# Kernel tuning notes

Hardware: AMD Instinct MI355X
Metric: run time of the kernel (lower is better)

## Reference

```python
import jax, jax.numpy as jnp
import numpy as np

MIDC = 256
HEADS = 8
HEADC = MIDC // HEADS
EPS = 1e-5


def _ln(x, gamma, beta):
    # LayerNorm over last dim (headc)
    mu = jnp.mean(x, axis=-1, keepdims=True)
    var = jnp.var(x, axis=-1, keepdims=True)
    return (x - mu) * jax.lax.rsqrt(var + EPS) * gamma + beta


def setup_inputs() -> dict:
    key = jax.random.key(0)
    ks = jax.random.split(key, 8)
    B, HW, C = 8, 4096, MIDC
    s = 1.0 / np.sqrt(C)
    return {
        "x": jax.random.normal(ks[0], (B, HW, C), jnp.float32),
        "w_qkv": jax.random.normal(ks[1], (C, 3 * C), jnp.float32) * s,
        "b_qkv": jnp.zeros((3 * C,), jnp.float32),
        "kln_g": jnp.ones((HEADC,), jnp.float32),
        "kln_b": jnp.zeros((HEADC,), jnp.float32),
        "vln_g": jnp.ones((HEADC,), jnp.float32),
        "vln_b": jnp.zeros((HEADC,), jnp.float32),
        "w1": jax.random.normal(ks[2], (C, C), jnp.float32) * s,
        "b1": jnp.zeros((C,), jnp.float32),
        "w2": jax.random.normal(ks[3], (C, C), jnp.float32) * s,
        "b2": jnp.zeros((C,), jnp.float32),
    }


def reference(x, w_qkv, b_qkv, kln_g, kln_b, vln_g, vln_b, w1, b1, w2, b2):
    B, HW, C = x.shape
    bias = x
    qkv = (x @ w_qkv + b_qkv).reshape(B, HW, HEADS, 3 * HEADC)
    qkv = qkv.transpose(0, 2, 1, 3)  # [B, h, HW, 3*headc]
    q, k, v = jnp.split(qkv, 3, axis=-1)  # each [B, h, HW, headc]
    k = _ln(k, kln_g, kln_b)
    v = _ln(v, vln_g, vln_b)
    # linear attention: (k^T v)/HW then q @ (.)
    kv = jnp.einsum('bhnd,bhne->bhde', k, v) / HW  # [B, h, headc, headc]
    out = jnp.einsum('bhnd,bhde->bhne', q, kv)     # [B, h, HW, headc]
    out = out.transpose(0, 2, 1, 3).reshape(B, HW, C)
    ret = out + bias
    # GELU MLP (torch nn.GELU default = exact erf form)
    h = jax.nn.gelu(ret @ w1 + b1, approximate=False)
    return h @ w2 + b2 + bias
```

## Files before the change

### kernel.cpp

```cpp
#include <hip/hip_runtime.h>
#include <hip/hip_bf16.h>
#include <math.h>

typedef _Float16 f16;
typedef _Float16 f16x4 __attribute__((ext_vector_type(4)));
typedef _Float16 f16x8 __attribute__((ext_vector_type(8)));
typedef float f32x4 __attribute__((ext_vector_type(4)));

#define MIDC 256
#define NHEADS 8
#define HEADC 32
#define HW_ 4096
#define BATCH 8
#define NTOK (BATCH*HW_)

__device__ __forceinline__ void gload_lds16(const void* g, void* lds){
    __builtin_amdgcn_global_load_lds(
        (const __attribute__((address_space(1))) unsigned int*)g,
        (__attribute__((address_space(3))) unsigned int*)lds, 16, 0, 0);
}

__global__ void k_f32_to_f16(const float* __restrict__ in, f16* __restrict__ out, int n){
    int i = (blockIdx.x*blockDim.x + threadIdx.x)*4;
    if (i < n) {
        float4 v = *reinterpret_cast<const float4*>(in + i);
        f16x4 o = { (f16)v.x, (f16)v.y, (f16)v.z, (f16)v.w };
        *reinterpret_cast<f16x4*>(out + i) = o;
    }
}

__global__ void k_prep(const float* __restrict__ wqkv, const float* __restrict__ w1,
                       const float* __restrict__ w2, const float* __restrict__ bq,
                       f16* __restrict__ wqkvT, f16* __restrict__ w1T,
                       f16* __restrict__ w2T, float* __restrict__ pb){
    int idx = blockIdx.x*blockDim.x + threadIdx.x;
    if (idx < 196608){
        int r = idx / 768, o = idx % 768;
        int h = o / 96, rr = o % 96, p = rr >> 5, d = o & 31;
        int n = (p << 8) + (h << 5) + d;
        wqkvT[(size_t)n*256 + r] = (f16)wqkv[idx];
    } else if (idx < 262144){
        int i = idx - 196608; int r = i >> 8, c = i & 255;
        w1T[(size_t)c*256 + r] = (f16)w1[i];
    } else if (idx < 327680){
        int i = idx - 262144; int r = i >> 8, c = i & 255;
        w2T[(size_t)c*256 + r] = (f16)w2[i];
    } else if (idx < 328448){
        int n = idx - 327680;
        int p = n >> 8, h = (n & 255) >> 5, d = n & 31;
        pb[n] = bq[h*96 + p*32 + d];
    }
}

__global__ __launch_bounds__(256) void k_gemm0(
    const f16* __restrict__ A, const f16* __restrict__ Bt,
    const float* __restrict__ bias,
    const float* __restrict__ kg_, const float* __restrict__ kb_,
    const float* __restrict__ vg_, const float* __restrict__ vb_,
    f16* __restrict__ oq, f16* __restrict__ ok, f16* __restrict__ ov)
{
    constexpr int K = 256;
    __shared__ __attribute__((aligned(16))) char smem[50176];
    f16* const AsB[2] = { (f16*)(smem),        (f16*)(smem+16384) };
    f16* const BsB[2] = { (f16*)(smem+8192),   (f16*)(smem+24576) };

    const int tid  = threadIdx.x;
    const int lane = tid & 63, wid = tid >> 6;

    const int nwg  = 6 * 256;
    const int orig = blockIdx.x + 6*blockIdx.y;
    const int lin  = (orig & 7) * (nwg >> 3) + (orig >> 3);
    const int bx = lin % 6, by = lin / 6;
    const int m0 = by * 128, n0 = bx * 128;

    const int wm = (wid >> 1) * 64, wn = (wid & 1) * 64;
    const int lr = lane & 15, kg = lane >> 4;

    f32x4 acc[4][4];
    #pragma unroll
    for (int i=0;i<4;i++)
        #pragma unroll
        for (int j=0;j<4;j++) acc[i][j] = (f32x4){0.f,0.f,0.f,0.f};

    const int srow = tid >> 2, scol = (tid & 3) * 8;
    const f16* gA = A  + (size_t)(m0 + srow)*K + scol;
    const f16* gB = Bt + (size_t)(n0 + srow)*K + scol;
    const size_t rstep = (size_t)64*K;

    auto STAGE = [&](int b, int kt){
        f16* ab = AsB[b] + wid*512;
        f16* bb = BsB[b] + wid*512;
        gload_lds16(gA + kt,          ab);
        gload_lds16(gA + kt + rstep,  ab + 2048);
        gload_lds16(gB + kt,          bb);
        gload_lds16(gB + kt + rstep,  bb + 2048);
    };

    STAGE(0, 0);
    __syncthreads();
    #pragma unroll
    for (int t = 0; t < 8; ++t){
        const int cur = t & 1;
        if (t < 7) STAGE(cur ^ 1, (t+1)*32);
        const f16* Ac = AsB[cur];
        const f16* Bc = BsB[cur];
        f16x8 a[4], b[4];
        #pragma unroll
        for (int fr=0; fr<4; fr++) a[fr] = *reinterpret_cast<const f16x8*>(Ac + (wm + fr*16 + lr)*32 + kg*8);
        #pragma unroll
        for (int fc=0; fc<4; fc++) b[fc] = *reinterpret_cast<const f16x8*>(Bc + (wn + fc*16 + lr)*32 + kg*8);
        #pragma unroll
        for (int fr=0; fr<4; fr++)
            #pragma unroll
            for (int fc=0; fc<4; fc++)
                acc[fr][fc] = __builtin_amdgcn_mfma_f32_16x16x32_f16(a[fr], b[fc], acc[fr][fc], 0, 0, 0);
        __syncthreads();
    }

    f16* Cs = (f16*)(smem + 16384);
    float bv[4];
    #pragma unroll
    for (int fc=0; fc<4; fc++) bv[fc] = bias[n0 + wn + fc*16 + lr];
    #pragma unroll
    for (int fr=0; fr<4; fr++)
    #pragma unroll
    for (int fc=0; fc<4; fc++)
    #pragma unroll
    for (int r=0; r<4; r++){
        float v = acc[fr][fc][r] + bv[fc];
        Cs[(wm + fr*16 + kg*4 + r)*132 + (wn + fc*16 + lr)] = (f16)v;
    }
    __syncthreads();
    int part = n0 >> 8;
    #pragma unroll
    for (int i=0;i<2;i++){
        int c = tid + i*256;
        int row = c >> 2, hc = c & 3;
        const f16* src = Cs + row*132 + hc*32;
        f16x8 d0 = *reinterpret_cast<const f16x8*>(src);
        f16x8 d1 = *reinterpret_cast<const f16x8*>(src + 8);
        f16x8 d2 = *reinterpret_cast<const f16x8*>(src + 16);
        f16x8 d3 = *reinterpret_cast<const f16x8*>(src + 24);
        int col0 = n0 + hc*32;
        int h = (col0 & 255) >> 5;
        int gm = m0 + row, b = gm >> 12, n = gm & 4095;
        f16* dst = (part==0 ? oq : (part==1 ? ok : ov))
                 + ((size_t)(b*NHEADS + h)*HW_ + n)*HEADC;
        if (part == 0){
            *reinterpret_cast<f16x8*>(dst)      = d0;
            *reinterpret_cast<f16x8*>(dst + 8)  = d1;
            *reinterpret_cast<f16x8*>(dst + 16) = d2;
            *reinterpret_cast<f16x8*>(dst + 24) = d3;
        } else {
            float vals[32];
            #pragma unroll
            for (int j=0;j<8;j++){
                vals[j]    = (float)d0[j];
                vals[8+j]  = (float)d1[j];
                vals[16+j] = (float)d2[j];
                vals[24+j] = (float)d3[j];
            }
            float s = 0.f, s2 = 0.f;
            #pragma unroll
            for (int j=0;j<32;j++){ s += vals[j]; s2 = fmaf(vals[j], vals[j], s2); }
            float mu  = s * (1.0f/32.0f);
            float var = s2 * (1.0f/32.0f) - mu*mu;
            float rs  = rsqrtf(var + 1e-5f);
            const float* gp = (part==1) ? kg_ : vg_;
            const float* bp = (part==1) ? kb_ : vb_;
            f16x8 o0, o1, o2, o3;
            #pragma unroll
            for (int j=0;j<8;j++){
                o0[j] = (f16)((vals[j]    - mu)*rs*gp[j]    + bp[j]);
                o1[j] = (f16)((vals[8+j]  - mu)*rs*gp[8+j]  + bp[8+j]);
                o2[j] = (f16)((vals[16+j] - mu)*rs*gp[16+j] + bp[16+j]);
                o3[j] = (f16)((vals[24+j] - mu)*rs*gp[24+j] + bp[24+j]);
            }
            *reinterpret_cast<f16x8*>(dst)      = o0;
            *reinterpret_cast<f16x8*>(dst + 8)  = o1;
            *reinterpret_cast<f16x8*>(dst + 16) = o2;
            *reinterpret_cast<f16x8*>(dst + 24) = o3;
        }
    }
}

template<int MODE>
__global__ __launch_bounds__(256, 4) void k_mlp(
    const f16* __restrict__ A, const f16* __restrict__ Bt,
    const float* __restrict__ bias,
    f16* __restrict__ oh,
    const f16* __restrict__ residh, float* __restrict__ of)
{
    constexpr int K = 256;
    __shared__ __attribute__((aligned(16))) char smem[24576];

    const int tid  = threadIdx.x;
    const int lane = tid & 63, wid = tid >> 6;

    const int nwg  = 4 * 256;
    const int orig = blockIdx.x + 4*blockIdx.y;
    const int lin  = (orig & 7) * (nwg >> 3) + (orig >> 3);
    const int bx = lin & 3, by = lin >> 2;
    const int m0 = by * 128, n0 = bx * 64;

    const int wm = (wid >> 1) * 64;
    const int wn = (wid & 1) * 32;
    const int lr = lane & 15, kg = lane >> 4;

    f32x4 acc[4][2];
    #pragma unroll
    for (int i=0;i<4;i++)
        #pragma unroll
        for (int j=0;j<2;j++) acc[i][j] = (f32x4){0.f,0.f,0.f,0.f};

    const int srow = tid >> 2, scol = (tid & 3) * 8;
    const f16* gA = A  + (size_t)(m0 + srow)*K + scol;
    const f16* gB = Bt + (size_t)(n0 + srow)*K + scol;

    auto STAGE = [&](int b, int kt){
        f16* Ab = (f16*)(smem + b*12288);
        f16* Bb = Ab + 4096;
        gload_lds16(gA + kt,                 Ab + wid*512);
        gload_lds16(gA + kt + (size_t)64*K,  Ab + 2048 + wid*512);
        gload_lds16(gB + kt,                 Bb + wid*512);
    };

    STAGE(0, 0);
    __syncthreads();
    #pragma unroll
    for (int t = 0; t < 8; ++t){
        const int cur = t & 1;
        if (t < 7) STAGE(cur ^ 1, (t+1)*32);
        const f16* Ab = (const f16*)(smem + cur*12288);
        const f16* Bb = Ab + 4096;
        f16x8 a[4], bf[2];
        #pragma unroll
        for (int fr=0; fr<4; fr++) a[fr]  = *reinterpret_cast<const f16x8*>(Ab + (wm + fr*16 + lr)*32 + kg*8);
        #pragma unroll
        for (int fc=0; fc<2; fc++) bf[fc] = *reinterpret_cast<const f16x8*>(Bb + (wn + fc*16 + lr)*32 + kg*8);
        #pragma unroll
        for (int fr=0; fr<4; fr++)
            #pragma unroll
            for (int fc=0; fc<2; fc++)
                acc[fr][fc] = __builtin_amdgcn_mfma_f32_16x16x32_f16(a[fr], bf[fc], acc[fr][fc], 0, 0, 0);
        __syncthreads();
    }

    float bv[2];
    #pragma unroll
    for (int fc=0; fc<2; fc++) bv[fc] = bias[n0 + wn + fc*16 + lr];

    if constexpr (MODE == 1){
        f16* Cs = (f16*)smem;
        #pragma unroll
        for (int fr=0; fr<4; fr++)
        #pragma unroll
        for (int fc=0; fc<2; fc++)
        #pragma unroll
        for (int r=0; r<4; r++){
            float v = acc[fr][fc][r] + bv[fc];
            v = 0.5f * v * (1.0f + erff(v * 0.70710678f));
            Cs[(wm + fr*16 + kg*4 + r)*72 + (wn + fc*16 + lr)] = (f16)v;
        }
        __syncthreads();
        int row = tid >> 1, ch = tid & 1;
        const f16* src = Cs + row*72 + ch*32;
        f16x8 d0 = *reinterpret_cast<const f16x8*>(src);
        f16x8 d1 = *reinterpret_cast<const f16x8*>(src + 8);
        f16x8 d2 = *reinterpret_cast<const f16x8*>(src + 16);
        f16x8 d3 = *reinterpret_cast<const f16x8*>(src + 24);
        f16* dst = oh + (size_t)(m0 + row)*MIDC + n0 + ch*32;
        *reinterpret_cast<f16x8*>(dst)      = d0;
        *reinterpret_cast<f16x8*>(dst + 8)  = d1;
        *reinterpret_cast<f16x8*>(dst + 16) = d2;
        *reinterpret_cast<f16x8*>(dst + 24) = d3;
    } else {
        #pragma unroll
        for (int fr=0; fr<4; fr++)
        #pragma unroll
        for (int fc=0; fc<2; fc++)
        #pragma unroll
        for (int r=0; r<4; r++){
            int gm = m0 + wm + fr*16 + kg*4 + r;
            int gn = n0 + wn + fc*16 + lr;
            size_t xi = (size_t)gm*MIDC + gn;
            of[xi] = acc[fr][fc][r] + bv[fc] + (float)residh[xi];
        }
    }
}

__global__ __launch_bounds__(256) void k_kv(const f16* __restrict__ kb, const f16* __restrict__ vb,
                                            float* __restrict__ kvpart){
    __shared__ __attribute__((aligned(16))) f16 ks[4][64][32];
    __shared__ __attribute__((aligned(16))) f16 vs[4][64][32];
    __shared__ __attribute__((aligned(16))) float red[4][32][32];
    const int bh = blockIdx.x, chunk = blockIdx.y;
    const int tid = threadIdx.x, lane = tid & 63, wid = tid >> 6;
    const int d0 = (lane >> 3) * 4, e0 = (lane & 7) * 4;
    const int tok0 = chunk*256 + wid*64;

    const f16* kg = kb + ((size_t)bh*HW_ + tok0)*HEADC;
    const f16* vg = vb + ((size_t)bh*HW_ + tok0)*HEADC;
    f16* ksw = &ks[wid][0][0]; f16* vsw = &vs[wid][0][0];
    #pragma unroll
    for (int i=0;i<4;i++){
        gload_lds16(kg + (size_t)(i*16 + (lane>>2))*HEADC + (lane&3)*8, ksw + i*512);
        gload_lds16(vg + (size_t)(i*16 + (lane>>2))*HEADC + (lane&3)*8, vsw + i*512);
    }
    __syncthreads();

    f32x4 acc[4];
    #pragma unroll
    for (int i=0;i<4;i++) acc[i] = (f32x4){0.f,0.f,0.f,0.f};
    #pragma unroll 4
    for (int t=0; t<64; t++){
        f16x4 kk = *reinterpret_cast<const f16x4*>(&ks[wid][t][d0]);
        f16x4 vv = *reinterpret_cast<const f16x4*>(&vs[wid][t][e0]);
        f32x4 vf = { (float)vv[0], (float)vv[1], (float)vv[2], (float)vv[3] };
        #pragma unroll
        for (int i=0;i<4;i++) acc[i] += (float)kk[i] * vf;
    }
    __syncthreads();
    #pragma unroll
    for (int i=0;i<4;i++) *reinterpret_cast<f32x4*>(&red[wid][d0+i][e0]) = acc[i];
    __syncthreads();
    int de0 = tid * 4;
    const float* rf = &red[0][0][0];
    f32x4 s = *reinterpret_cast<const f32x4*>(rf + de0);
    #pragma unroll
    for (int w=1; w<4; w++) s += *reinterpret_cast<const f32x4*>(rf + w*1024 + de0);
    *reinterpret_cast<f32x4*>(kvpart + ((size_t)bh*16 + chunk)*1024 + de0) = s;
}

__global__ void k_kvred(const float* __restrict__ kvpart, f16* __restrict__ kvT){
    int gid = blockIdx.x*blockDim.x + threadIdx.x;
    int bh = gid >> 10, de = gid & 1023;
    int d = de >> 5, e = de & 31;
    float s = 0.f;
    #pragma unroll
    for (int p=0; p<16; p++) s += kvpart[((size_t)bh*16 + p)*1024 + de];
    kvT[((size_t)bh << 10) + (e << 5) + d] = (f16)(s * (1.0f/4096.0f));
}

__global__ __launch_bounds__(256) void k_attn(const f16* __restrict__ qb, const f16* __restrict__ kvT,
                                              const f16* __restrict__ xb, f16* __restrict__ ret){
    __shared__ __attribute__((aligned(16))) f16 Ls[128][40];
    const int bh = blockIdx.x, chunk = blockIdx.y;
    const int b = bh >> 3, h = bh & 7;
    const int tid = threadIdx.x, lane = tid & 63, wid = tid >> 6;
    const int lr = lane & 15, kg = lane >> 4;
    const int row0 = chunk*128 + wid*32;

    f32x4 acc[2][2];
    #pragma unroll
    for (int i=0;i<2;i++)
        #pragma unroll
        for (int j=0;j<2;j++) acc[i][j] = (f32x4){0.f,0.f,0.f,0.f};

    f16x8 a[2], bb[2];
    #pragma unroll
    for (int fr=0; fr<2; fr++)
        a[fr] = *reinterpret_cast<const f16x8*>(qb + ((size_t)bh*HW_ + row0 + fr*16 + lr)*HEADC + kg*8);
    #pragma unroll
    for (int fc=0; fc<2; fc++)
        bb[fc] = *reinterpret_cast<const f16x8*>(kvT + ((size_t)bh << 10) + (size_t)(fc*16 + lr)*32 + kg*8);
    #pragma unroll
    for (int fr=0; fr<2; fr++)
        #pragma unroll
        for (int fc=0; fc<2; fc++)
            acc[fr][fc] = __builtin_amdgcn_mfma_f32_16x16x32_f16(a[fr], bb[fc], acc[fr][fc], 0, 0, 0);

    #pragma unroll
    for (int fr=0; fr<2; fr++)
    #pragma unroll
    for (int fc=0; fc<2; fc++)
    #pragma unroll
    for (int r=0; r<4; r++)
        Ls[wid*32 + fr*16 + kg*4 + r][fc*16 + lr] = (f16)acc[fr][fc][r];
    __syncthreads();

    int row = tid >> 1, hf = tid & 1;
    size_t base = ((size_t)b*HW_ + chunk*128 + row)*MIDC + h*HEADC + hf*16;
    f16x8 x0 = *reinterpret_cast<const f16x8*>(xb + base);
    f16x8 x1 = *reinterpret_cast<const f16x8*>(xb + base + 8);
    f16x8 s0 = *reinterpret_cast<const f16x8*>(&Ls[row][hf*16]);
    f16x8 s1 = *reinterpret_cast<const f16x8*>(&Ls[row][hf*16 + 8]);
    f16x8 o0, o1;
    #pragma unroll
    for (int j=0;j<8;j++){
        o0[j] = (f16)((float)s0[j] + (float)x0[j]);
        o1[j] = (f16)((float)s1[j] + (float)x1[j]);
    }
    *reinterpret_cast<f16x8*>(ret + base)     = o0;
    *reinterpret_cast<f16x8*>(ret + base + 8) = o1;
}

extern "C" void kernel_launch(void* const* d_in, const int* in_sizes, int n_in,
                              void* d_out, int out_size, void* d_ws, size_t ws_size,
                              hipStream_t stream) {
    const float* x     = (const float*)d_in[0];
    const float* w_qkv = (const float*)d_in[1];
    const float* b_qkv = (const float*)d_in[2];
    const float* kln_g = (const float*)d_in[3];
    const float* kln_b = (const float*)d_in[4];
    const float* vln_g = (const float*)d_in[5];
    const float* vln_b = (const float*)d_in[6];
    const float* w1    = (const float*)d_in[7];
    const float* b1    = (const float*)d_in[8];
    const float* w2    = (const float*)d_in[9];
    const float* b2    = (const float*)d_in[10];
    float* out = (float*)d_out;

    char* ws = (char*)d_ws;
    size_t off = 0;
    auto alloc = [&](size_t bytes) -> void* {
        void* p = ws + off; off += (bytes + 255) & ~255ULL; return p;
    };
    const size_t TOKB = (size_t)NTOK*MIDC*sizeof(f16);
    f16* xb    = (f16*)alloc(TOKB);
    f16* wqkvT = (f16*)alloc(768*256*sizeof(f16));
    f16* w1T   = (f16*)alloc(256*256*sizeof(f16));
    f16* w2T   = (f16*)alloc(256*256*sizeof(f16));
    float* pb  = (float*)alloc(768*sizeof(float));
    f16* qb    = (f16*)alloc(TOKB);
    f16* kb    = (f16*)alloc(TOKB);
    f16* vb    = (f16*)alloc(TOKB);
    float* kvpart = (float*)alloc((size_t)64*16*1024*sizeof(float));
    f16* kvT   = (f16*)alloc((size_t)64*1024*sizeof(f16));
    f16* retb = vb;
    f16* hb   = kb;

    k_f32_to_f16<<<dim3((NTOK*MIDC)/4/256), 256, 0, stream>>>(x, xb, NTOK*MIDC);
    k_prep<<<dim3((328448+255)/256), 256, 0, stream>>>(w_qkv, w1, w2, b_qkv, wqkvT, w1T, w2T, pb);

    k_gemm0<<<dim3(6, NTOK/128), 256, 0, stream>>>(
        xb, wqkvT, pb, kln_g, kln_b, vln_g, vln_b, qb, kb, vb);

    k_kv<<<dim3(64, HW_/256), 256, 0, stream>>>(kb, vb, kvpart);
    k_kvred<<<dim3(65536/256), 256, 0, stream>>>(kvpart, kvT);

    k_attn<<<dim3(64, HW_/128), 256, 0, stream>>>(qb, kvT, xb, retb);

    k_mlp<1><<<dim3(4, NTOK/128), 256, 0, stream>>>(
        retb, w1T, b1, hb, nullptr, nullptr);

    k_mlp<2><<<dim3(4, NTOK/128), 256, 0, stream>>>(
        hb, w2T, b2, nullptr, xb, out);
}
```

Measured before the change: 200.0 us.

## Merge prep kernels, fold kv reduction into attention, shrink LDS footprint

Combines the x conversion and weight-prep kernels into one launch, and removes the separate kv reduction kernel by having each attention block sum the 16 partial kv tiles itself into LDS. It also shrinks LDS in the QKV GEMM (epilogue staged in two halves reusing the operand buffers) and in k_kv (reduction buffer aliased over operand storage) to allow more resident workgroups. The aim is fewer launches and higher occupancy. The cost is that each attention block redundantly re-reads and reduces 64KB of partials (32 blocks per head), and the GEMM epilogue gains an extra barrier.

Result: faster. 193.7 us (-3.2%).

```diff
diff --git a/kernel.cpp b/kernel.cpp
--- a/kernel.cpp
+++ b/kernel.cpp
@@ -20,35 +20,35 @@
         (__attribute__((address_space(3))) unsigned int*)lds, 16, 0, 0);
 }
 
-__global__ void k_f32_to_f16(const float* __restrict__ in, f16* __restrict__ out, int n){
-    int i = (blockIdx.x*blockDim.x + threadIdx.x)*4;
-    if (i < n) {
-        float4 v = *reinterpret_cast<const float4*>(in + i);
+__global__ void k_init(const float* __restrict__ x, const float* __restrict__ wqkv,
+                       const float* __restrict__ w1, const float* __restrict__ w2,
+                       const float* __restrict__ bq,
+                       f16* __restrict__ xb, f16* __restrict__ wqkvT,
+                       f16* __restrict__ w1T, f16* __restrict__ w2T, float* __restrict__ pb){
+    int t = blockIdx.x*blockDim.x + threadIdx.x;
+    if (t < 2097152){
+        int i = t*4;
+        float4 v = *reinterpret_cast<const float4*>(x + i);
         f16x4 o = { (f16)v.x, (f16)v.y, (f16)v.z, (f16)v.w };
-        *reinterpret_cast<f16x4*>(out + i) = o;
-    }
-}
-
-__global__ void k_prep(const float* __restrict__ wqkv, const float* __restrict__ w1,
-                       const float* __restrict__ w2, const float* __restrict__ bq,
-                       f16* __restrict__ wqkvT, f16* __restrict__ w1T,
-                       f16* __restrict__ w2T, float* __restrict__ pb){
-    int idx = blockIdx.x*blockDim.x + threadIdx.x;
-    if (idx < 196608){
-        int r = idx / 768, o = idx % 768;
-        int h = o / 96, rr = o % 96, p = rr >> 5, d = o & 31;
-        int n = (p << 8) + (h << 5) + d;
-        wqkvT[(size_t)n*256 + r] = (f16)wqkv[idx];
-    } else if (idx < 262144){
-        int i = idx - 196608; int r = i >> 8, c = i & 255;
-        w1T[(size_t)c*256 + r] = (f16)w1[i];
-    } else if (idx < 327680){
-        int i = idx - 262144; int r = i >> 8, c = i & 255;
-        w2T[(size_t)c*256 + r] = (f16)w2[i];
-    } else if (idx < 328448){
-        int n = idx - 327680;
-        int p = n >> 8, h = (n & 255) >> 5, d = n & 31;
-        pb[n] = bq[h*96 + p*32 + d];
+        *reinterpret_cast<f16x4*>(xb + i) = o;
+    } else {
+        int j = t - 2097152;
+        if (j < 196608){
+            int r = j / 768, o = j % 768;
+            int h = o / 96, rr = o % 96, p = rr >> 5, d = o & 31;
+            int n = (p << 8) + (h << 5) + d;
+            wqkvT[(size_t)n*256 + r] = (f16)wqkv[j];
+        } else if (j < 262144){
+            int i2 = j - 196608; int r = i2 >> 8, c = i2 & 255;
+            w1T[(size_t)c*256 + r] = (f16)w1[i2];
+        } else if (j < 327680){
+            int i2 = j - 262144; int r = i2 >> 8, c = i2 & 255;
+            w2T[(size_t)c*256 + r] = (f16)w2[i2];
+        } else if (j < 328448){
+            int n = j - 327680;
+            int p = n >> 8, h = (n & 255) >> 5, d = n & 31;
+            pb[n] = bq[h*96 + p*32 + d];
+        }
     }
 }
 
@@ -60,9 +60,7 @@
     f16* __restrict__ oq, f16* __restrict__ ok, f16* __restrict__ ov)
 {
     constexpr int K = 256;
-    __shared__ __attribute__((aligned(16))) char smem[50176];
-    f16* const AsB[2] = { (f16*)(smem),        (f16*)(smem+16384) };
-    f16* const BsB[2] = { (f16*)(smem+8192),   (f16*)(smem+24576) };
+    __shared__ __attribute__((aligned(16))) char smem[32768];
 
     const int tid  = threadIdx.x;
     const int lane = tid & 63, wid = tid >> 6;
@@ -88,8 +86,9 @@
     const size_t rstep = (size_t)64*K;
 
     auto STAGE = [&](int b, int kt){
-        f16* ab = AsB[b] + wid*512;
-        f16* bb = BsB[b] + wid*512;
+        f16* base = (f16*)smem + b*8192;
+        f16* ab = base + wid*512;
+        f16* bb = base + 4096 + wid*512;
         gload_lds16(gA + kt,          ab);
         gload_lds16(gA + kt + rstep,  ab + 2048);
         gload_lds16(gB + kt,          bb);
@@ -102,8 +101,8 @@
     for (int t = 0; t < 8; ++t){
         const int cur = t & 1;
         if (t < 7) STAGE(cur ^ 1, (t+1)*32);
-        const f16* Ac = AsB[cur];
-        const f16* Bc = BsB[cur];
+        const f16* Ac = (const f16*)smem + cur*8192;
+        const f16* Bc = Ac + 4096;
         f16x8 a[4], b[4];
         #pragma unroll
         for (int fr=0; fr<4; fr++) a[fr] = *reinterpret_cast<const f16x8*>(Ac + (wm + fr*16 + lr)*32 + kg*8);
@@ -117,33 +116,36 @@
         __syncthreads();
     }
 
-    f16* Cs = (f16*)(smem + 16384);
+    f16* Cs = (f16*)smem;
     float bv[4];
     #pragma unroll
     for (int fc=0; fc<4; fc++) bv[fc] = bias[n0 + wn + fc*16 + lr];
-    #pragma unroll
-    for (int fr=0; fr<4; fr++)
-    #pragma unroll
-    for (int fc=0; fc<4; fc++)
-    #pragma unroll
-    for (int r=0; r<4; r++){
-        float v = acc[fr][fc][r] + bv[fc];
-        Cs[(wm + fr*16 + kg*4 + r)*132 + (wn + fc*16 + lr)] = (f16)v;
-    }
-    __syncthreads();
-    int part = n0 >> 8;
-    #pragma unroll
-    for (int i=0;i<2;i++){
-        int c = tid + i*256;
-        int row = c >> 2, hc = c & 3;
+    const int part = n0 >> 8;
+    #pragma unroll
+    for (int half=0; half<2; ++half){
+        if (half) __syncthreads();
+        if ((wid >> 1) == half){
+            #pragma unroll
+            for (int fr=0; fr<4; fr++)
+            #pragma unroll
+            for (int fc=0; fc<4; fc++)
+            #pragma unroll
+            for (int r=0; r<4; r++){
+                float v = acc[fr][fc][r] + bv[fc];
+                Cs[(fr*16 + kg*4 + r)*132 + (wn + fc*16 + lr)] = (f16)v;
+            }
+        }
+        __syncthreads();
+        int row = tid >> 2, hc = tid & 3;
         const f16* src = Cs + row*132 + hc*32;
         f16x8 d0 = *reinterpret_cast<const f16x8*>(src);
         f16x8 d1 = *reinterpret_cast<const f16x8*>(src + 8);
         f16x8 d2 = *reinterpret_cast<const f16x8*>(src + 16);
         f16x8 d3 = *reinterpret_cast<const f16x8*>(src + 24);
+        int gm = m0 + half*64 + row;
         int col0 = n0 + hc*32;
         int h = (col0 & 255) >> 5;
-        int gm = m0 + row, b = gm >> 12, n = gm & 4095;
+        int b = gm >> 12, n = gm & 4095;
         f16* dst = (part==0 ? oq : (part==1 ? ok : ov))
                  + ((size_t)(b*NHEADS + h)*HW_ + n)*HEADC;
         if (part == 0){
@@ -291,9 +293,10 @@
 
 __global__ __launch_bounds__(256) void k_kv(const f16* __restrict__ kb, const f16* __restrict__ vb,
                                             float* __restrict__ kvpart){
-    __shared__ __attribute__((aligned(16))) f16 ks[4][64][32];
-    __shared__ __attribute__((aligned(16))) f16 vs[4][64][32];
-    __shared__ __attribute__((aligned(16))) float red[4][32][32];
+    __shared__ __attribute__((aligned(16))) char sm[32768];
+    f16* ks = (f16*)sm;
+    f16* vs = (f16*)(sm + 16384);
+    float* red = (float*)sm;
     const int bh = blockIdx.x, chunk = blockIdx.y;
     const int tid = threadIdx.x, lane = tid & 63, wid = tid >> 6;
     const int d0 = (lane >> 3) * 4, e0 = (lane & 7) * 4;
@@ -301,7 +304,7 @@
 
     const f16* kg = kb + ((size_t)bh*HW_ + tok0)*HEADC;
     const f16* vg = vb + ((size_t)bh*HW_ + tok0)*HEADC;
-    f16* ksw = &ks[wid][0][0]; f16* vsw = &vs[wid][0][0];
+    f16* ksw = ks + wid*2048; f16* vsw = vs + wid*2048;
     #pragma unroll
     for (int i=0;i<4;i++){
         gload_lds16(kg + (size_t)(i*16 + (lane>>2))*HEADC + (lane&3)*8, ksw + i*512);
@@ -314,36 +317,26 @@
     for (int i=0;i<4;i++) acc[i] = (f32x4){0.f,0.f,0.f,0.f};
     #pragma unroll 4
     for (int t=0; t<64; t++){
-        f16x4 kk = *reinterpret_cast<const f16x4*>(&ks[wid][t][d0]);
-        f16x4 vv = *reinterpret_cast<const f16x4*>(&vs[wid][t][e0]);
+        f16x4 kk = *reinterpret_cast<const f16x4*>(ks + wid*2048 + t*32 + d0);
+        f16x4 vv = *reinterpret_cast<const f16x4*>(vs + wid*2048 + t*32 + e0);
         f32x4 vf = { (float)vv[0], (float)vv[1], (float)vv[2], (float)vv[3] };
         #pragma unroll
         for (int i=0;i<4;i++) acc[i] += (float)kk[i] * vf;
     }
     __syncthreads();
     #pragma unroll
-    for (int i=0;i<4;i++) *reinterpret_cast<f32x4*>(&red[wid][d0+i][e0]) = acc[i];
+    for (int i=0;i<4;i++) *reinterpret_cast<f32x4*>(red + wid*1024 + (d0+i)*32 + e0) = acc[i];
     __syncthreads();
     int de0 = tid * 4;
-    const float* rf = &red[0][0][0];
-    f32x4 s = *reinterpret_cast<const f32x4*>(rf + de0);
-    #pragma unroll
-    for (int w=1; w<4; w++) s += *reinterpret_cast<const f32x4*>(rf + w*1024 + de0);
+    f32x4 s = *reinterpret_cast<const f32x4*>(red + de0);
+    #pragma unroll
+    for (int w=1; w<4; w++) s += *reinterpret_cast<const f32x4*>(red + w*1024 + de0);
     *reinterpret_cast<f32x4*>(kvpart + ((size_t)bh*16 + chunk)*1024 + de0) = s;
 }
 
-__global__ void k_kvred(const float* __restrict__ kvpart, f16* __restrict__ kvT){
-    int gid = blockIdx.x*blockDim.x + threadIdx.x;
-    int bh = gid >> 10, de = gid & 1023;
-    int d = de >> 5, e = de & 31;
-    float s = 0.f;
-    #pragma unroll
-    for (int p=0; p<16; p++) s += kvpart[((size_t)bh*16 + p)*1024 + de];
-    kvT[((size_t)bh << 10) + (e << 5) + d] = (f16)(s * (1.0f/4096.0f));
-}
-
-__global__ __launch_bounds__(256) void k_attn(const f16* __restrict__ qb, const f16* __restrict__ kvT,
+__global__ __launch_bounds__(256) void k_attn(const f16* __restrict__ qb, const float* __restrict__ kvpart,
                                               const f16* __restrict__ xb, f16* __restrict__ ret){
+    __shared__ __attribute__((aligned(16))) f16 kvs[32][40];
     __shared__ __attribute__((aligned(16))) f16 Ls[128][40];
     const int bh = blockIdx.x, chunk = blockIdx.y;
     const int b = bh >> 3, h = bh & 7;
@@ -351,6 +344,18 @@
     const int lr = lane & 15, kg = lane >> 4;
     const int row0 = chunk*128 + wid*32;
 
+    {
+        int de0 = tid * 4;
+        const float* base = kvpart + (size_t)bh*16384 + de0;
+        f32x4 s = *reinterpret_cast<const f32x4*>(base);
+        #pragma unroll
+        for (int p=1; p<16; p++) s += *reinterpret_cast<const f32x4*>(base + p*1024);
+        int d = de0 >> 5, e0 = de0 & 31;
+        #pragma unroll
+        for (int j=0;j<4;j++) kvs[e0+j][d] = (f16)(s[j] * (1.0f/4096.0f));
+    }
+    __syncthreads();
+
     f32x4 acc[2][2];
     #pragma unroll
     for (int i=0;i<2;i++)
@@ -363,7 +368,7 @@
         a[fr] = *reinterpret_cast<const f16x8*>(qb + ((size_t)bh*HW_ + row0 + fr*16 + lr)*HEADC + kg*8);
     #pragma unroll
     for (int fc=0; fc<2; fc++)
-        bb[fc] = *reinterpret_cast<const f16x8*>(kvT + ((size_t)bh << 10) + (size_t)(fc*16 + lr)*32 + kg*8);
+        bb[fc] = *reinterpret_cast<const f16x8*>(&kvs[fc*16 + lr][kg*8]);
     #pragma unroll
     for (int fr=0; fr<2; fr++)
         #pragma unroll
@@ -426,20 +431,17 @@
     f16* kb    = (f16*)alloc(TOKB);
     f16* vb    = (f16*)alloc(TOKB);
     float* kvpart = (float*)alloc((size_t)64*16*1024*sizeof(float));
-    f16* kvT   = (f16*)alloc((size_t)64*1024*sizeof(f16));
     f16* retb = vb;
     f16* hb   = kb;
 
-    k_f32_to_f16<<<dim3((NTOK*MIDC)/4/256), 256, 0, stream>>>(x, xb, NTOK*MIDC);
-    k_prep<<<dim3((328448+255)/256), 256, 0, stream>>>(w_qkv, w1, w2, b_qkv, wqkvT, w1T, w2T, pb);
+    k_init<<<dim3(9475), 256, 0, stream>>>(x, w_qkv, w1, w2, b_qkv, xb, wqkvT, w1T, w2T, pb);
 
     k_gemm0<<<dim3(6, NTOK/128), 256, 0, stream>>>(
         xb, wqkvT, pb, kln_g, kln_b, vln_g, vln_b, qb, kb, vb);
 
     k_kv<<<dim3(64, HW_/256), 256, 0, stream>>>(kb, vb, kvpart);
-    k_kvred<<<dim3(65536/256), 256, 0, stream>>>(kvpart, kvT);
-
-    k_attn<<<dim3(64, HW_/128), 256, 0, stream>>>(qb, kvT, xb, retb);
+
+    k_attn<<<dim3(64, HW_/128), 256, 0, stream>>>(qb, kvpart, xb, retb);
 
     k_mlp<1><<<dim3(4, NTOK/128), 256, 0, stream>>>(
         retb, w1T, b1, hb, nullptr, nullptr);
```
